# Performance work log

Measured on AMD Instinct MI355X. Metric: run time of the kernel, lower is better.

Reference implementation:

```python
import jax, jax.numpy as jnp
import numpy as np
from jax import lax

B, T, D, V, K = 32, 2048, 512, 1024, 3
COVERAGE_FLOOR = 0.05
LN_EPS = 1e-5


def _gelu(x):
    return jax.nn.gelu(x, approximate=False)  # torch F.gelu default is exact erf


def _causal_conv(h, w, b):
    # h: [B,T,D]; w: [D_out, D_in, K]; left-pad (K-1) for causality
    x = jnp.transpose(h, (0, 2, 1))  # [B,D,T]
    y = lax.conv_general_dilated(x, w, window_strides=(1,),
                                 padding=[(w.shape[-1] - 1, 0)],
                                 dimension_numbers=("NCH", "OIH", "NCH"))
    return jnp.transpose(y + b[None, :, None], (0, 2, 1))  # [B,T,D]


def _layer_norm(x, g, b):
    m = x.mean(-1, keepdims=True)
    v = ((x - m) ** 2).mean(-1, keepdims=True)
    return (x - m) / jnp.sqrt(v + LN_EPS) * g + b


def _masked_median(values, mask):
    # values, mask: [B,T]; torch median = lower middle = sorted[(n-1)//2]
    valid = mask > 0.5
    n = valid.sum(axis=1)  # [B]
    s = jnp.sort(jnp.where(valid, values, jnp.inf), axis=1)
    idx = jnp.clip((n - 1) // 2, 0, values.shape[1] - 1)
    med = jnp.take_along_axis(s, idx[:, None], axis=1)  # [B,1]
    return jnp.where((n > 0)[:, None], med, 0.0)


def _masked_mean(values, mask):
    denom = jnp.clip(mask.sum(axis=1, keepdims=True), 1.0, None)  # [B,1]
    return (values * mask[:, :, None]).sum(axis=1) / denom  # [B,D]


def _masked_std(values, mask, mean):
    denom = jnp.clip(mask.sum(axis=1, keepdims=True), 1.0, None)
    diff2 = (values - mean[:, None, :]) ** 2 * mask[:, :, None]
    return jnp.sqrt(diff2.sum(axis=1) / jnp.clip(denom, 1e-6, None) + 1e-6)


def setup_inputs() -> dict:
    key = jax.random.key(0)
    ks = jax.random.split(key, 16)
    s = 0.02
    return {
        "unit_ids": jax.random.randint(ks[0], (B, T), 0, V),
        "duration_obs": jax.random.uniform(ks[1], (B, T), jnp.float32, 0.01, 2.0),
        "mask": (jax.random.uniform(ks[2], (B, T)) > 0.3).astype(jnp.float32),
        "emb": jax.random.normal(ks[3], (V, D), jnp.float32) * s,
        "aux_w": jax.random.normal(ks[4], (D, 1), jnp.float32) * s,
        "aux_b": jnp.zeros((D,), jnp.float32),
        "conv1_w": jax.random.normal(ks[5], (D, D, K), jnp.float32) * s,
        "conv1_b": jnp.zeros((D,), jnp.float32),
        "conv2_w": jax.random.normal(ks[6], (D, D, K), jnp.float32) * s,
        "conv2_b": jnp.zeros((D,), jnp.float32),
        "ln_g": jnp.ones((D,), jnp.float32),
        "ln_b": jnp.zeros((D,), jnp.float32),
        "p1_w": jax.random.normal(ks[7], (D, 2 * D), jnp.float32) * s,
        "p1_b": jnp.zeros((D,), jnp.float32),
        "p2_w": jax.random.normal(ks[8], (D, D), jnp.float32) * s,
        "p2_b": jnp.zeros((D,), jnp.float32),
    }


def reference(unit_ids, duration_obs, mask, emb, aux_w, aux_b,
              conv1_w, conv1_b, conv2_w, conv2_b, ln_g, ln_b,
              p1_w, p1_b, p2_w, p2_b):
    mask = jnp.clip(mask.astype(jnp.float32), 0.0, 1.0)  # [B,T]
    logdur = jnp.log(jnp.clip(duration_obs.astype(jnp.float32), 1e-4, None)) * mask
    global_rate = _masked_median(logdur, mask)  # [B,1]
    ref_residual = (logdur - global_rate) * mask  # [B,T]

    # CausalStretchQueryEncoder
    hidden = emb[unit_ids] + (ref_residual[:, :, None] * aux_w[None, None, :, 0] + aux_b)
    hidden = _gelu(_causal_conv(hidden, conv1_w, conv1_b))
    hidden = _gelu(_causal_conv(hidden, conv2_w, conv2_b))
    hidden = _layer_norm(hidden, ln_g, ln_b) * mask[:, :, None]  # [B,T,D]

    mean = _masked_mean(hidden, mask)  # [B,D]
    std = _masked_std(hidden, mask, mean)  # [B,D]
    h = jnp.concatenate([mean, std], axis=-1)  # [B,2D]
    summary_state = jnp.tanh(_gelu(h @ p1_w.T + p1_b) @ p2_w.T + p2_b)  # [B,D]

    support_raw = mask.sum(axis=1, keepdims=True)  # [B,1]
    support = jnp.clip(support_raw, 1.0, None)
    summary_state = jnp.where(support_raw > 0.0, summary_state, 0.0)
    coverage = jnp.clip(support_raw / float(T), COVERAGE_FLOOR, None)

    residual_mean = (ref_residual * mask).sum(axis=1, keepdims=True) / support  # [B,1]
    residual_var = jnp.clip(((ref_residual - residual_mean) ** 2 * mask).sum(axis=1, keepdims=True) / support, 1e-4, None)
    attn = (mask / support)[:, :, None]  # [B,T,1]
    prompt_role_fit = residual_mean * jnp.ones_like(ref_residual) * mask  # [B,T]
    coeff_norm = jnp.linalg.norm(summary_state, axis=-1, keepdims=True)  # [B,1]

    return (global_rate, summary_state, residual_mean, residual_var, coverage,
            mask, logdur, ref_residual, attn, prompt_role_fit, coeff_norm)
```

## Files before the change

kernel.cpp:

```cpp
#include <hip/hip_runtime.h>
#include <hip/hip_bf16.h>
#include <math.h>

#define B_  32
#define T_  2048
#define D_  512
#define V_  1024
#define K_  3

typedef __attribute__((ext_vector_type(8))) short   short8;
typedef __attribute__((ext_vector_type(4))) float   floatx4;
typedef __attribute__((ext_vector_type(2))) long    longx2;

#define SCALE_H0 256.0f
#define SCALE_A  64.0f
#define SCALE_W  16.0f
#define INV1 (1.0f/(SCALE_H0*SCALE_W))
#define INV2 (1.0f/(SCALE_A*SCALE_W))

#define OFF0 0
#define OFF1 32
#define OFF2 16416
#define OFF3 16448
#define OFF4 16480
#define OFF5 16512
#define OFF6 82048
#define OFF7 147584
#define OFF8 213120
#define OFF9 278656
#define OFF10 344192

#define WS_RR     0
#define WS_SUP    262144
#define WS_PSUM   262272
#define WS_PSUMSQ 327808
#define WS_W1P    393344
#define WS_W2P    1212544
#define WS_H1     2031744
#define WS_S1     35618944
#define WS_NRM    35684480

__device__ __forceinline__ float clampf(float v, float lo, float hi) {
    v = (v > lo) ? v : lo;
    return (v < hi) ? v : hi;
}
__device__ __forceinline__ float gelu_exact(float v) {
    return 0.5f * v * (1.0f + erff(v * 0.70710678118654752440f));
}
__device__ __forceinline__ unsigned char f2fp8(float x) {
    int v = __builtin_amdgcn_cvt_pk_fp8_f32(x, x, 0, false);
    return (unsigned char)(v & 0xFF);
}
__device__ __forceinline__ int pk4fp8(float a, float b, float c, float d) {
    int p0 = __builtin_amdgcn_cvt_pk_fp8_f32(a, b, 0, false);
    int p1 = __builtin_amdgcn_cvt_pk_fp8_f32(c, d, 0, false);
    return (p1 << 16) | (p0 & 0xFFFF);
}

__device__ __forceinline__ float block_reduce_sum(float v, float* red, int tid) {
    __syncthreads();
    red[tid] = v;
    __syncthreads();
    for (int s = 128; s > 0; s >>= 1) {
        if (tid < s) red[tid] += red[tid + s];
        __syncthreads();
    }
    float r = red[0];
    __syncthreads();
    return r;
}

#define NB 2048
#define HLO (-9.3f)
#define HSC ((float)NB / 10.05f)
#define WLS 1544
__global__ __launch_bounds__(256) void init_kernel(
    const float* __restrict__ dur, const float* __restrict__ maskp,
    const float* __restrict__ w1, const float* __restrict__ w2,
    unsigned char* __restrict__ W1p, unsigned char* __restrict__ W2p,
    unsigned char* __restrict__ H1buf,
    float* __restrict__ rr_ws, float* __restrict__ sup_ws,
    float* __restrict__ psum, float* __restrict__ out)
{
    int tid = threadIdx.x;

    if (blockIdx.x >= 32) {
        __shared__ unsigned char Wl[2 * 16 * WLS];
        int ntg = blockIdx.x - 32;
        int lane = tid & 63, wave = tid >> 6;

        #pragma unroll
        for (int ws = 0; ws < 2; ++ws) {
            const float* wsrc = (ws ? w2 : w1) + (size_t)ntg * 16 * 1536;
            for (int i = tid; i < 6144; i += 256) {
                float4 v = ((const float4*)wsrc)[i];
                int col_local = i / 384;
                int pos = (i % 384) * 4;
                int word = pk4fp8(v.x * SCALE_W, v.y * SCALE_W,
                                  v.z * SCALE_W, v.w * SCALE_W);
                *(int*)(&Wl[(ws * 16 + col_local) * WLS + pos]) = word;
            }
        }
        __syncthreads();

        int cl = lane & 15, qq = lane >> 4;
        int pg = ntg >> 1, half = ntg & 1;
        #pragma unroll
        for (int ws = 0; ws < 2; ++ws) {
            unsigned char* dst = ws ? W2p : W1p;
            for (int s = wave; s < 48; s += 4) {
                int ci = s & 15, k = s >> 4;
                const unsigned char* row = &Wl[(ws * 16 + cl) * WLS];
                int kin = ci * 32 + qq * 8;
                unsigned char bb[8];
                #pragma unroll
                for (int e = 0; e < 8; ++e)
                    bb[e] = row[(kin + e) * 3 + k];
                *(double*)(dst + (((size_t)(s * 16 + pg) * 64 + lane) * 16
                                  + half * 8)) = *(double*)bb;
            }
        }

        int pid2 = ntg * 256 + tid;
        #pragma unroll
        for (int j = 0; j < 4; ++j) {
            int idx = pid2 + j * 8192;
            psum[idx] = 0.0f;
            int b = idx >> 10;
            int r = (idx >> 9) & 1;
            int d = idx & 511;
            H1buf[((size_t)b * 2050 + r) * 512 + d] = 0;
        }
        return;
    }

    __shared__ int   hist[NB];
    __shared__ int   csum[256];
    __shared__ float red[256];
    __shared__ float cand[128];
    __shared__ float nsh, medsh;
    __shared__ int   sh_tb, sh_cb, sh_candn;

    int b = blockIdx.x;
    const float* durb = dur + (size_t)b * T_;
    const float* mkb  = maskp + (size_t)b * T_;

    float ld[8], mk[8];
    int   bn[8];
    float cnt = 0.0f;
    #pragma unroll
    for (int i = 0; i < 8; ++i) hist[tid * 8 + i] = 0;
    __syncthreads();
    #pragma unroll
    for (int i = 0; i < 8; ++i) {
        int t = tid + i * 256;
        float m = clampf(mkb[t], 0.0f, 1.0f);
        float dv = durb[t];
        dv = (dv >= 1e-4f) ? dv : 1e-4f;
        float l = logf(dv) * m;
        ld[i] = l; mk[i] = m;
        int bin = (int)((l - HLO) * HSC);
        bin = (bin < 0) ? 0 : ((bin > NB - 1) ? NB - 1 : bin);
        bn[i] = bin;
        if (m > 0.5f) { cnt += 1.0f; atomicAdd(&hist[bin], 1); }
    }
    float n = block_reduce_sum(cnt, red, tid);
    if (tid == 0) { nsh = n; sh_candn = 0; medsh = 0.0f; }

    {
        int cs = 0;
        #pragma unroll
        for (int i = 0; i < 8; ++i) cs += hist[tid * 8 + i];
        csum[tid] = cs;
        __syncthreads();
        for (int off = 1; off < 256; off <<= 1) {
            int v = (tid >= off) ? csum[tid - off] : 0;
            __syncthreads();
            csum[tid] += v;
            __syncthreads();
        }
    }
    int ni = (int)(n + 0.5f);
    int k  = (ni > 0) ? ((ni - 1) >> 1) : 0;
    {
        int prevIncl = (tid > 0) ? csum[tid - 1] : 0;
        if (ni > 0 && k >= prevIncl && k < csum[tid]) {
            int cum = prevIncl, tb = tid * 8;
            #pragma unroll
            for (int i = 0; i < 8; ++i) {
                int c = hist[tid * 8 + i];
                if (k < cum + c) { tb = tid * 8 + i; break; }
                cum += c;
            }
            sh_tb = tb; sh_cb = cum;
        }
    }
    __syncthreads();
    if (ni > 0) {
        int tb = sh_tb;
        #pragma unroll
        for (int i = 0; i < 8; ++i) {
            if (mk[i] > 0.5f && bn[i] == tb) {
                int p = atomicAdd(&sh_candn, 1);
                if (p < 128) cand[p] = ld[i];
            }
        }
    }
    __syncthreads();
    if (tid == 0 && ni > 0) {
        int m = k - sh_cb;
        int cn = (sh_candn < 128) ? sh_candn : 128;
        float best = cand[0];
        for (int i = 0; i < cn; ++i) {
            int rank = 0;
            for (int j = 0; j < cn; ++j)
                rank += (cand[j] < cand[i]) || (cand[j] == cand[i] && j < i);
            if (rank == m) { best = cand[i]; break; }
        }
        medsh = best;
    }
    __syncthreads();
    float med = (ni > 0) ? medsh : 0.0f;
    med = clampf(med, -20.0f, 20.0f);

    float denom = (n > 1.0f) ? n : 1.0f;
    float rv[8];
    float ssum = 0.0f;
    #pragma unroll
    for (int i = 0; i < 8; ++i) { rv[i] = (ld[i] - med) * mk[i]; ssum += rv[i]; }
    float rsum = block_reduce_sum(ssum, red, tid);
    float rm = clampf(rsum / denom, -40.0f, 40.0f);

    float vsum_l = 0.0f;
    #pragma unroll
    for (int i = 0; i < 8; ++i) { float dd = rv[i] - rm; vsum_l += dd * dd * mk[i]; }
    float vsum = block_reduce_sum(vsum_l, red, tid);
    float var = clampf(vsum / denom, 1e-4f, 1e4f);

    float inv_sup = 1.0f / denom;
    #pragma unroll
    for (int i = 0; i < 8; ++i) {
        int t = tid + i * 256;
        size_t o = (size_t)b * T_ + t;
        out[OFF5 + o] = mk[i];
        out[OFF6 + o] = ld[i];
        out[OFF7 + o] = rv[i];
        out[OFF8 + o] = mk[i] * inv_sup;
        out[OFF9 + o] = rm * mk[i];
        rr_ws[o] = rv[i];
    }
    if (tid == 0) {
        out[OFF0 + b] = med;
        out[OFF2 + b] = rm;
        out[OFF3 + b] = var;
        float cov = n * (1.0f / (float)T_);
        out[OFF4 + b] = (cov > 0.05f) ? cov : 0.05f;
        sup_ws[b] = n;
    }
}

#define H0S 520
__global__ __launch_bounds__(256, 3) void conv1g_kernel(
    const int* __restrict__ ids, const float* __restrict__ rr,
    const float* __restrict__ emb,
    const float* __restrict__ aux_w, const float* __restrict__ aux_b,
    const unsigned char* __restrict__ W1p, const float* __restrict__ bias1,
    unsigned char* __restrict__ H1buf)
{
    __shared__ __align__(16) unsigned char H0s[66 * H0S];
    __shared__ int   lid[66];
    __shared__ float lrr[66];

    int tile = blockIdx.x;
    int b    = blockIdx.y;
    int r0   = tile << 6;
    int tid  = threadIdx.x;
    int wave = tid >> 6, lane = tid & 63;
    int q = lane >> 4, m16 = lane & 15;

    if (tid < 66) {
        int t = r0 - 2 + tid;
        bool v = (t >= 0);
        lid[tid] = v ? ids[b * T_ + t] : -1;
        lrr[tid] = v ? rr[(size_t)b * T_ + t] : 0.0f;
    }
    __syncthreads();

    {
        int c4 = tid & 127;
        float4 aw = *(const float4*)(aux_w + c4 * 4);
        float4 ab = *(const float4*)(aux_b + c4 * 4);
        int rbase = tid >> 7;
        for (int j = 0; j < 33; ++j) {
            int row = rbase + j * 2;
            int id = lid[row];
            int word = 0;
            if (id >= 0) {
                float vr = lrr[row];
                float4 e = *(const float4*)(emb + (size_t)id * D_ + c4 * 4);
                word = pk4fp8((e.x + vr * aw.x + ab.x) * SCALE_H0,
                              (e.y + vr * aw.y + ab.y) * SCALE_H0,
                              (e.z + vr * aw.z + ab.z) * SCALE_H0,
                              (e.w + vr * aw.w + ab.w) * SCALE_H0);
            }
            *(int*)(&H0s[row * H0S + c4 * 4]) = word;
        }
    }
    __syncthreads();

    unsigned char* Ob = H1buf + ((size_t)b * 2050 + 2 + r0) * 512;

#define CONV1_PHASE(FR0, FR1, SS)                                              \
    {   int k1 = (SS) >> 4, ci = (SS) & 15;                                    \
        _Pragma("unroll")                                                      \
        for (int mt = 0; mt < 4; ++mt) {                                       \
            long afr = *(const long*)(&H0s[(mt * 16 + m16 + k1) * H0S + ci * 32 + q * 8]); \
            acc[mt][0] = __builtin_amdgcn_mfma_f32_16x16x32_fp8_fp8(afr, FR0[0], acc[mt][0], 0, 0, 0); \
            acc[mt][1] = __builtin_amdgcn_mfma_f32_16x16x32_fp8_fp8(afr, FR0[1], acc[mt][1], 0, 0, 0); \
            acc[mt][2] = __builtin_amdgcn_mfma_f32_16x16x32_fp8_fp8(afr, FR1[0], acc[mt][2], 0, 0, 0); \
            acc[mt][3] = __builtin_amdgcn_mfma_f32_16x16x32_fp8_fp8(afr, FR1[1], acc[mt][3], 0, 0, 0); \
        } }

    #pragma unroll
    for (int nh = 0; nh < 2; ++nh) {
        floatx4 acc[4][4];
        #pragma unroll
        for (int i = 0; i < 4; ++i)
            #pragma unroll
            for (int j = 0; j < 4; ++j)
                acc[i][j] = (floatx4){0.f, 0.f, 0.f, 0.f};

        const longx2* wp0 = (const longx2*)W1p
                          + ((size_t)(0 * 16 + nh * 8 + wave * 2 + 0) * 64 + lane);
        const longx2* wp1 = wp0 + 64;

        longx2 fA0 = wp0[0],                  fA1 = wp1[0];
        longx2 fB0 = wp0[(size_t)1 * 1024],   fB1 = wp1[(size_t)1 * 1024];
        longx2 fC0, fC1, fD0, fD1;

        #pragma unroll 1
        for (int s = 0; s < 48; s += 4) {
            fC0 = wp0[(size_t)(s + 2) * 1024]; fC1 = wp1[(size_t)(s + 2) * 1024];
            CONV1_PHASE(fA0, fA1, s)
            fD0 = wp0[(size_t)(s + 3) * 1024]; fD1 = wp1[(size_t)(s + 3) * 1024];
            CONV1_PHASE(fB0, fB1, s + 1)
            fA0 = wp0[(size_t)(s + 4) * 1024]; fA1 = wp1[(size_t)(s + 4) * 1024];
            CONV1_PHASE(fC0, fC1, s + 2)
            fB0 = wp0[(size_t)(s + 5) * 1024]; fB1 = wp1[(size_t)(s + 5) * 1024];
            CONV1_PHASE(fD0, fD1, s + 3)
        }

        #pragma unroll
        for (int mt = 0; mt < 4; ++mt) {
            #pragma unroll
            for (int nt = 0; nt < 4; ++nt) {
                int col = nh * 256 + wave * 64 + nt * 16 + m16;
                float bsv = bias1[col];
                #pragma unroll
                for (int r = 0; r < 4; ++r) {
                    int row = mt * 16 + q * 4 + r;
                    float v = gelu_exact(acc[mt][nt][r] * INV1 + bsv) * SCALE_A;
                    Ob[(size_t)row * 512 + col] = f2fp8(v);
                }
            }
        }
    }
#undef CONV1_PHASE
}

#define H1S 520
__global__ __launch_bounds__(256, 2) void conv2ln_kernel(
    const unsigned char* __restrict__ H1buf, const unsigned char* __restrict__ W2p,
    const float* __restrict__ bias2,
    const float* __restrict__ ln_g, const float* __restrict__ ln_b,
    const float* __restrict__ maskp,
    float* __restrict__ psum, float* __restrict__ psumsq)
{
    __shared__ __align__(16) unsigned char H1s[34 * H1S];
    __shared__ float mrow[32];
    __shared__ float part[32][4][2];
    __shared__ float tot[32][2];
    __shared__ float colsum[512][2];

    int tile = blockIdx.x;
    int b    = blockIdx.y;
    int r0   = tile << 5;
    int tid  = threadIdx.x;
    int wave = tid >> 6, lane = tid & 63;
    int q = lane >> 4, m16 = lane & 15;
    int nbase = wave << 7;

    const unsigned char* src = H1buf + ((size_t)b * 2050 + r0) * 512;
    for (int g = tid; g < 34 * 32; g += 256) {
        int row = g >> 5, h = g & 31;
        *(float4*)(&H1s[row * H1S + h * 16]) = *(const float4*)(src + (size_t)row * 512 + h * 16);
    }
    if (tid < 32)
        mrow[tid] = clampf(maskp[(size_t)b * T_ + r0 + tid], 0.0f, 1.0f);
    __syncthreads();

    floatx4 acc[2][8];
    #pragma unroll
    for (int i = 0; i < 2; ++i)
        #pragma unroll
        for (int j = 0; j < 8; ++j)
            acc[i][j] = (floatx4){0.f, 0.f, 0.f, 0.f};

    const longx2* wq0 = (const longx2*)W2p + ((size_t)(wave * 4 + 0) * 64 + lane);
    const longx2* wq1 = (const longx2*)W2p + ((size_t)(wave * 4 + 1) * 64 + lane);
    const longx2* wq2 = (const longx2*)W2p + ((size_t)(wave * 4 + 2) * 64 + lane);
    const longx2* wq3 = (const longx2*)W2p + ((size_t)(wave * 4 + 3) * 64 + lane);

#define C2_PHASE(F0, F1, F2, F3, SS)                                           \
    {   int k2 = (SS) >> 4, ci = (SS) & 15;                                    \
        _Pragma("unroll")                                                      \
        for (int mt = 0; mt < 2; ++mt) {                                       \
            long afr = *(const long*)(&H1s[(mt * 16 + m16 + k2) * H1S + ci * 32 + q * 8]); \
            acc[mt][0] = __builtin_amdgcn_mfma_f32_16x16x32_fp8_fp8(afr, F0[0], acc[mt][0], 0, 0, 0); \
            acc[mt][1] = __builtin_amdgcn_mfma_f32_16x16x32_fp8_fp8(afr, F0[1], acc[mt][1], 0, 0, 0); \
            acc[mt][2] = __builtin_amdgcn_mfma_f32_16x16x32_fp8_fp8(afr, F1[0], acc[mt][2], 0, 0, 0); \
            acc[mt][3] = __builtin_amdgcn_mfma_f32_16x16x32_fp8_fp8(afr, F1[1], acc[mt][3], 0, 0, 0); \
            acc[mt][4] = __builtin_amdgcn_mfma_f32_16x16x32_fp8_fp8(afr, F2[0], acc[mt][4], 0, 0, 0); \
            acc[mt][5] = __builtin_amdgcn_mfma_f32_16x16x32_fp8_fp8(afr, F2[1], acc[mt][5], 0, 0, 0); \
            acc[mt][6] = __builtin_amdgcn_mfma_f32_16x16x32_fp8_fp8(afr, F3[0], acc[mt][6], 0, 0, 0); \
            acc[mt][7] = __builtin_amdgcn_mfma_f32_16x16x32_fp8_fp8(afr, F3[1], acc[mt][7], 0, 0, 0); \
        } }

    longx2 fA0 = wq0[0], fA1 = wq1[0], fA2 = wq2[0], fA3 = wq3[0];
    longx2 fB0 = wq0[(size_t)1 * 1024], fB1 = wq1[(size_t)1 * 1024];
    longx2 fB2 = wq2[(size_t)1 * 1024], fB3 = wq3[(size_t)1 * 1024];
    longx2 fC0, fC1, fC2, fC3, fD0, fD1, fD2, fD3;

    #pragma unroll 1
    for (int s = 0; s < 48; s += 4) {
        fC0 = wq0[(size_t)(s + 2) * 1024]; fC1 = wq1[(size_t)(s + 2) * 1024];
        fC2 = wq2[(size_t)(s + 2) * 1024]; fC3 = wq3[(size_t)(s + 2) * 1024];
        C2_PHASE(fA0, fA1, fA2, fA3, s)
        fD0 = wq0[(size_t)(s + 3) * 1024]; fD1 = wq1[(size_t)(s + 3) * 1024];
        fD2 = wq2[(size_t)(s + 3) * 1024]; fD3 = wq3[(size_t)(s + 3) * 1024];
        C2_PHASE(fB0, fB1, fB2, fB3, s + 1)
        fA0 = wq0[(size_t)(s + 4) * 1024]; fA1 = wq1[(size_t)(s + 4) * 1024];
        fA2 = wq2[(size_t)(s + 4) * 1024]; fA3 = wq3[(size_t)(s + 4) * 1024];
        C2_PHASE(fC0, fC1, fC2, fC3, s + 2)
        fB0 = wq0[(size_t)(s + 5) * 1024]; fB1 = wq1[(size_t)(s + 5) * 1024];
        fB2 = wq2[(size_t)(s + 5) * 1024]; fB3 = wq3[(size_t)(s + 5) * 1024];
        C2_PHASE(fD0, fD1, fD2, fD3, s + 3)
    }
#undef C2_PHASE

    #pragma unroll
    for (int mt = 0; mt < 2; ++mt)
        #pragma unroll
        for (int nt = 0; nt < 8; ++nt) {
            int col = nbase + nt * 16 + m16;
            float bsv = bias2[col];
            #pragma unroll
            for (int r = 0; r < 4; ++r)
                acc[mt][nt][r] = gelu_exact(acc[mt][nt][r] * INV2 + bsv);
        }

    #pragma unroll
    for (int mt = 0; mt < 2; ++mt) {
        #pragma unroll
        for (int r = 0; r < 4; ++r) {
            float rs = 0.f, rq = 0.f;
            #pragma unroll
            for (int nt = 0; nt < 8; ++nt) {
                float v = acc[mt][nt][r];
                rs += v; rq += v * v;
            }
            rs += __shfl_xor(rs, 1);  rq += __shfl_xor(rq, 1);
            rs += __shfl_xor(rs, 2);  rq += __shfl_xor(rq, 2);
            rs += __shfl_xor(rs, 4);  rq += __shfl_xor(rq, 4);
            rs += __shfl_xor(rs, 8);  rq += __shfl_xor(rq, 8);
            if (m16 == 0) {
                int row = mt * 16 + q * 4 + r;
                part[row][wave][0] = rs;
                part[row][wave][1] = rq;
            }
        }
    }
    __syncthreads();
    if (tid < 64) {
        int row = tid >> 1, j = tid & 1;
        tot[row][j] = part[row][0][j] + part[row][1][j] + part[row][2][j] + part[row][3][j];
    }
    __syncthreads();

    float meanv[2][4], rstdv[2][4];
    #pragma unroll
    for (int mt = 0; mt < 2; ++mt)
        #pragma unroll
        for (int r = 0; r < 4; ++r) {
            int row = mt * 16 + q * 4 + r;
            float m = tot[row][0] * (1.0f / D_);
            float var = tot[row][1] * (1.0f / D_) - m * m;
            meanv[mt][r] = m;
            rstdv[mt][r] = rsqrtf((var > 0.0f ? var : 0.0f) + 1e-5f);
        }

    float cs[8], cq[8];
    #pragma unroll
    for (int nt = 0; nt < 8; ++nt) { cs[nt] = 0.f; cq[nt] = 0.f; }
    #pragma unroll
    for (int mt = 0; mt < 2; ++mt) {
        #pragma unroll
        for (int r = 0; r < 4; ++r) {
            int row = mt * 16 + q * 4 + r;
            float mk = mrow[row];
            float m = meanv[mt][r], rs = rstdv[mt][r];
            #pragma unroll
            for (int nt = 0; nt < 8; ++nt) {
                int col = nbase + nt * 16 + m16;
                float xn = ((acc[mt][nt][r] - m) * rs * ln_g[col] + ln_b[col]) * mk;
                cs[nt] += xn;
                cq[nt] += xn * xn;
            }
        }
    }
    #pragma unroll
    for (int nt = 0; nt < 8; ++nt) {
        cs[nt] += __shfl_xor(cs[nt], 16);  cq[nt] += __shfl_xor(cq[nt], 16);
        cs[nt] += __shfl_xor(cs[nt], 32);  cq[nt] += __shfl_xor(cq[nt], 32);
    }
    if (lane < 16) {
        #pragma unroll
        for (int nt = 0; nt < 8; ++nt) {
            int col = nbase + nt * 16 + m16;
            colsum[col][0] = cs[nt];
            colsum[col][1] = cq[nt];
        }
    }
    __syncthreads();
    for (int i = tid; i < 512; i += 256) {
        atomicAdd(&psum[(size_t)b * D_ + i], colsum[i][0]);
        atomicAdd(&psumsq[(size_t)b * D_ + i], colsum[i][1]);
    }
}

__global__ __launch_bounds__(128) void mlp1_kernel(
    const float* __restrict__ psum, const float* __restrict__ psumsq,
    const float* __restrict__ sup_ws,
    const float* __restrict__ p1w, const float* __restrict__ p1b,
    float* __restrict__ s1_ws, float* __restrict__ nrm_ws)
{
    int b = blockIdx.x, jt = blockIdx.y;
    int tid = threadIdx.x;
    __shared__ float h[2 * D_];

    float n = sup_ws[b];
    float denom = (n > 1.0f) ? n : 1.0f;
    for (int i = tid; i < D_; i += 128) {
        float S = psum[(size_t)b * D_ + i];
        float Q = psumsq[(size_t)b * D_ + i];
        float mean = S / denom;
        float msum = Q - 2.0f * mean * S + n * mean * mean;
        float arg = msum / denom + 1e-6f;
        h[i] = mean;
        h[D_ + i] = sqrtf((arg > 0.0f) ? arg : 0.0f);
    }
    if (jt == 0 && tid == 0) nrm_ws[b] = 0.0f;
    __syncthreads();

    int d  = jt * 64 + (tid >> 1);
    int kh = tid & 1;
    float z = (kh == 0) ? p1b[d] : 0.0f;
    const float4* w4 = (const float4*)(p1w + (size_t)d * (2 * D_) + kh * D_);
    const float*  hh = &h[kh * D_];
    for (int jj = 0; jj < D_ / 4; ++jj) {
        float4 wv = w4[jj];
        z += hh[jj * 4 + 0] * wv.x + hh[jj * 4 + 1] * wv.y
           + hh[jj * 4 + 2] * wv.z + hh[jj * 4 + 3] * wv.w;
    }
    z += __shfl_xor(z, 1);
    if (kh == 0) s1_ws[(size_t)b * D_ + d] = gelu_exact(z);
}

__global__ __launch_bounds__(128) void mlp2_kernel(
    const float* __restrict__ s1_ws, const float* __restrict__ sup_ws,
    const float* __restrict__ p2w, const float* __restrict__ p2b,
    float* __restrict__ nrm_ws, float* __restrict__ out)
{
    int b = blockIdx.x, jt = blockIdx.y;
    int tid = threadIdx.x;
    __shared__ float s1[D_];
    __shared__ float red[128];

    for (int i = tid; i < D_; i += 128) s1[i] = s1_ws[(size_t)b * D_ + i];
    __syncthreads();

    int d  = jt * 64 + (tid >> 1);
    int kh = tid & 1;
    float z2 = (kh == 0) ? p2b[d] : 0.0f;
    const float4* w24 = (const float4*)(p2w + (size_t)d * D_ + kh * 256);
    const float*  ss  = &s1[kh * 256];
    for (int jj = 0; jj < 64; ++jj) {
        float4 wv = w24[jj];
        z2 += ss[jj * 4 + 0] * wv.x + ss[jj * 4 + 1] * wv.y
            + ss[jj * 4 + 2] * wv.z + ss[jj * 4 + 3] * wv.w;
    }
    z2 += __shfl_xor(z2, 1);
    float nsup = sup_ws[b];
    float st = tanhf(z2);
    if (!(nsup > 0.0f)) st = 0.0f;
    if (kh == 0) out[OFF1 + (size_t)b * D_ + d] = st;

    red[tid] = (kh == 0) ? st * st : 0.0f;
    __syncthreads();
    for (int s = 64; s > 0; s >>= 1) {
        if (tid < s) red[tid] += red[tid + s];
        __syncthreads();
    }
    if (tid == 0) atomicAdd(&nrm_ws[b], red[0]);
}

__global__ __launch_bounds__(64) void mlp3_kernel(
    const float* __restrict__ nrm_ws, float* __restrict__ out)
{
    int b = threadIdx.x;
    if (b < B_) out[OFF10 + b] = sqrtf(nrm_ws[b]);
}

extern "C" void kernel_launch(void* const* d_in, const int* in_sizes, int n_in,
                              void* d_out, int out_size, void* d_ws, size_t ws_size,
                              hipStream_t stream) {
    (void)in_sizes; (void)n_in; (void)out_size; (void)ws_size;
    const int*   unit_ids = (const int*)d_in[0];
    const float* dur      = (const float*)d_in[1];
    const float* mask     = (const float*)d_in[2];
    const float* emb      = (const float*)d_in[3];
    const float* aux_w    = (const float*)d_in[4];
    const float* aux_b    = (const float*)d_in[5];
    const float* conv1_w  = (const float*)d_in[6];
    const float* conv1_b  = (const float*)d_in[7];
    const float* conv2_w  = (const float*)d_in[8];
    const float* conv2_b  = (const float*)d_in[9];
    const float* ln_g     = (const float*)d_in[10];
    const float* ln_b     = (const float*)d_in[11];
    const float* p1_w     = (const float*)d_in[12];
    const float* p1_b     = (const float*)d_in[13];
    const float* p2_w     = (const float*)d_in[14];
    const float* p2_b     = (const float*)d_in[15];
    float* out = (float*)d_out;

    char* ws = (char*)d_ws;
    float*          rr     = (float*)(ws + WS_RR);
    float*          sup    = (float*)(ws + WS_SUP);
    float*          psum   = (float*)(ws + WS_PSUM);
    float*          psumsq = (float*)(ws + WS_PSUMSQ);
    unsigned char*  W1p    = (unsigned char*)(ws + WS_W1P);
    unsigned char*  W2p    = (unsigned char*)(ws + WS_W2P);
    unsigned char*  H1buf  = (unsigned char*)(ws + WS_H1);
    float*          s1_ws  = (float*)(ws + WS_S1);
    float*          nrm_ws = (float*)(ws + WS_NRM);

    init_kernel<<<dim3(64), dim3(256), 0, stream>>>(
        dur, mask, conv1_w, conv2_w, W1p, W2p, H1buf, rr, sup, psum, out);
    conv1g_kernel<<<dim3(32, 32), dim3(256), 0, stream>>>(
        unit_ids, rr, emb, aux_w, aux_b, W1p, conv1_b, H1buf);
    conv2ln_kernel<<<dim3(64, 32), dim3(256), 0, stream>>>(
        H1buf, W2p, conv2_b, ln_g, ln_b, mask, psum, psumsq);
    mlp1_kernel<<<dim3(32, 8), dim3(128), 0, stream>>>(
        psum, psumsq, sup, p1_w, p1_b, s1_ws, nrm_ws);
    mlp2_kernel<<<dim3(32, 8), dim3(128), 0, stream>>>(
        s1_ws, sup, p2_w, p2_b, nrm_ws, out);
    mlp3_kernel<<<dim3(1), dim3(64), 0, stream>>>(nrm_ws, out);
}
```

Measured before the change: 321.7 us.

## Split weight packing across more blocks, raise conv2 occupancy, fold norm kernel

Weight packing in init now gives each block only one of the two weight tensors, so it runs on 64 packing blocks instead of 32 with half the shared memory each. The conv2+LayerNorm kernel drops its hand-written four-stage register prefetch pipeline for a simple loop unrolled by two, and raises its launch-bounds occupancy target from 2 to 3 blocks per SM. The final sqrt-norm kernel is removed: a per-batch counter lets the last mlp2 block finish the norm, saving one launch. Losing the explicit prefetch may expose global-load latency in conv2 unless the higher occupancy hides it.

```diff
diff --git a/kernel.cpp b/kernel.cpp
--- a/kernel.cpp
+++ b/kernel.cpp
@@ -39,6 +39,7 @@
 #define WS_H1     2031744
 #define WS_S1     35618944
 #define WS_NRM    35684480
+#define WS_CNT    35684608
 
 __device__ __forceinline__ float clampf(float v, float lo, float hi) {
     v = (v > lo) ? v : lo;
@@ -85,46 +86,41 @@
     int tid = threadIdx.x;
 
     if (blockIdx.x >= 32) {
-        __shared__ unsigned char Wl[2 * 16 * WLS];
-        int ntg = blockIdx.x - 32;
+        __shared__ unsigned char Wl[16 * WLS];
+        int pb  = blockIdx.x - 32;
+        int ws  = pb & 1;
+        int ntg = pb >> 1;
         int lane = tid & 63, wave = tid >> 6;
 
-        #pragma unroll
-        for (int ws = 0; ws < 2; ++ws) {
-            const float* wsrc = (ws ? w2 : w1) + (size_t)ntg * 16 * 1536;
-            for (int i = tid; i < 6144; i += 256) {
-                float4 v = ((const float4*)wsrc)[i];
-                int col_local = i / 384;
-                int pos = (i % 384) * 4;
-                int word = pk4fp8(v.x * SCALE_W, v.y * SCALE_W,
-                                  v.z * SCALE_W, v.w * SCALE_W);
-                *(int*)(&Wl[(ws * 16 + col_local) * WLS + pos]) = word;
-            }
+        const float* wsrc = (ws ? w2 : w1) + (size_t)ntg * 16 * 1536;
+        for (int i = tid; i < 6144; i += 256) {
+            float4 v = ((const float4*)wsrc)[i];
+            int col_local = i / 384;
+            int pos = (i % 384) * 4;
+            int word = pk4fp8(v.x * SCALE_W, v.y * SCALE_W,
+                              v.z * SCALE_W, v.w * SCALE_W);
+            *(int*)(&Wl[col_local * WLS + pos]) = word;
         }
         __syncthreads();
 
         int cl = lane & 15, qq = lane >> 4;
         int pg = ntg >> 1, half = ntg & 1;
-        #pragma unroll
-        for (int ws = 0; ws < 2; ++ws) {
-            unsigned char* dst = ws ? W2p : W1p;
-            for (int s = wave; s < 48; s += 4) {
-                int ci = s & 15, k = s >> 4;
-                const unsigned char* row = &Wl[(ws * 16 + cl) * WLS];
-                int kin = ci * 32 + qq * 8;
-                unsigned char bb[8];
-                #pragma unroll
-                for (int e = 0; e < 8; ++e)
-                    bb[e] = row[(kin + e) * 3 + k];
-                *(double*)(dst + (((size_t)(s * 16 + pg) * 64 + lane) * 16
-                                  + half * 8)) = *(double*)bb;
-            }
-        }
-
-        int pid2 = ntg * 256 + tid;
-        #pragma unroll
-        for (int j = 0; j < 4; ++j) {
-            int idx = pid2 + j * 8192;
+        unsigned char* dst = ws ? W2p : W1p;
+        for (int s = wave; s < 48; s += 4) {
+            int ci = s & 15, k = s >> 4;
+            const unsigned char* row = &Wl[cl * WLS];
+            int kin = ci * 32 + qq * 8;
+            unsigned char bb[8];
+            #pragma unroll
+            for (int e = 0; e < 8; ++e)
+                bb[e] = row[(kin + e) * 3 + k];
+            *(double*)(dst + (((size_t)(s * 16 + pg) * 64 + lane) * 16
+                              + half * 8)) = *(double*)bb;
+        }
+
+        #pragma unroll
+        for (int j = 0; j < 2; ++j) {
+            int idx = pb * 512 + j * 256 + tid;
             psum[idx] = 0.0f;
             int b = idx >> 10;
             int r = (idx >> 9) & 1;
@@ -369,7 +365,7 @@
 }
 
 #define H1S 520
-__global__ __launch_bounds__(256, 2) void conv2ln_kernel(
+__global__ __launch_bounds__(256, 3) void conv2ln_kernel(
     const unsigned char* __restrict__ H1buf, const unsigned char* __restrict__ W2p,
     const float* __restrict__ bias2,
     const float* __restrict__ ln_g, const float* __restrict__ ln_b,
@@ -406,47 +402,28 @@
         for (int j = 0; j < 8; ++j)
             acc[i][j] = (floatx4){0.f, 0.f, 0.f, 0.f};
 
-    const longx2* wq0 = (const longx2*)W2p + ((size_t)(wave * 4 + 0) * 64 + lane);
-    const longx2* wq1 = (const longx2*)W2p + ((size_t)(wave * 4 + 1) * 64 + lane);
-    const longx2* wq2 = (const longx2*)W2p + ((size_t)(wave * 4 + 2) * 64 + lane);
-    const longx2* wq3 = (const longx2*)W2p + ((size_t)(wave * 4 + 3) * 64 + lane);
-
-#define C2_PHASE(F0, F1, F2, F3, SS)                                           \
-    {   int k2 = (SS) >> 4, ci = (SS) & 15;                                    \
-        _Pragma("unroll")                                                      \
-        for (int mt = 0; mt < 2; ++mt) {                                       \
-            long afr = *(const long*)(&H1s[(mt * 16 + m16 + k2) * H1S + ci * 32 + q * 8]); \
-            acc[mt][0] = __builtin_amdgcn_mfma_f32_16x16x32_fp8_fp8(afr, F0[0], acc[mt][0], 0, 0, 0); \
-            acc[mt][1] = __builtin_amdgcn_mfma_f32_16x16x32_fp8_fp8(afr, F0[1], acc[mt][1], 0, 0, 0); \
-            acc[mt][2] = __builtin_amdgcn_mfma_f32_16x16x32_fp8_fp8(afr, F1[0], acc[mt][2], 0, 0, 0); \
-            acc[mt][3] = __builtin_amdgcn_mfma_f32_16x16x32_fp8_fp8(afr, F1[1], acc[mt][3], 0, 0, 0); \
-            acc[mt][4] = __builtin_amdgcn_mfma_f32_16x16x32_fp8_fp8(afr, F2[0], acc[mt][4], 0, 0, 0); \
-            acc[mt][5] = __builtin_amdgcn_mfma_f32_16x16x32_fp8_fp8(afr, F2[1], acc[mt][5], 0, 0, 0); \
-            acc[mt][6] = __builtin_amdgcn_mfma_f32_16x16x32_fp8_fp8(afr, F3[0], acc[mt][6], 0, 0, 0); \
-            acc[mt][7] = __builtin_amdgcn_mfma_f32_16x16x32_fp8_fp8(afr, F3[1], acc[mt][7], 0, 0, 0); \
-        } }
-
-    longx2 fA0 = wq0[0], fA1 = wq1[0], fA2 = wq2[0], fA3 = wq3[0];
-    longx2 fB0 = wq0[(size_t)1 * 1024], fB1 = wq1[(size_t)1 * 1024];
-    longx2 fB2 = wq2[(size_t)1 * 1024], fB3 = wq3[(size_t)1 * 1024];
-    longx2 fC0, fC1, fC2, fC3, fD0, fD1, fD2, fD3;
-
-    #pragma unroll 1
-    for (int s = 0; s < 48; s += 4) {
-        fC0 = wq0[(size_t)(s + 2) * 1024]; fC1 = wq1[(size_t)(s + 2) * 1024];
-        fC2 = wq2[(size_t)(s + 2) * 1024]; fC3 = wq3[(size_t)(s + 2) * 1024];
-        C2_PHASE(fA0, fA1, fA2, fA3, s)
-        fD0 = wq0[(size_t)(s + 3) * 1024]; fD1 = wq1[(size_t)(s + 3) * 1024];
-        fD2 = wq2[(size_t)(s + 3) * 1024]; fD3 = wq3[(size_t)(s + 3) * 1024];
-        C2_PHASE(fB0, fB1, fB2, fB3, s + 1)
-        fA0 = wq0[(size_t)(s + 4) * 1024]; fA1 = wq1[(size_t)(s + 4) * 1024];
-        fA2 = wq2[(size_t)(s + 4) * 1024]; fA3 = wq3[(size_t)(s + 4) * 1024];
-        C2_PHASE(fC0, fC1, fC2, fC3, s + 2)
-        fB0 = wq0[(size_t)(s + 5) * 1024]; fB1 = wq1[(size_t)(s + 5) * 1024];
-        fB2 = wq2[(size_t)(s + 5) * 1024]; fB3 = wq3[(size_t)(s + 5) * 1024];
-        C2_PHASE(fD0, fD1, fD2, fD3, s + 3)
-    }
-#undef C2_PHASE
+    const longx2* wq = (const longx2*)W2p + ((size_t)(wave * 4) * 64 + lane);
+
+    #pragma unroll 2
+    for (int s = 0; s < 48; ++s) {
+        int k2 = s >> 4, ci = s & 15;
+        longx2 f0 = wq[(size_t)s * 1024];
+        longx2 f1 = wq[(size_t)s * 1024 + 64];
+        longx2 f2 = wq[(size_t)s * 1024 + 128];
+        longx2 f3 = wq[(size_t)s * 1024 + 192];
+        #pragma unroll
+        for (int mt = 0; mt < 2; ++mt) {
+            long afr = *(const long*)(&H1s[(mt * 16 + m16 + k2) * H1S + ci * 32 + q * 8]);
+            acc[mt][0] = __builtin_amdgcn_mfma_f32_16x16x32_fp8_fp8(afr, f0[0], acc[mt][0], 0, 0, 0);
+            acc[mt][1] = __builtin_amdgcn_mfma_f32_16x16x32_fp8_fp8(afr, f0[1], acc[mt][1], 0, 0, 0);
+            acc[mt][2] = __builtin_amdgcn_mfma_f32_16x16x32_fp8_fp8(afr, f1[0], acc[mt][2], 0, 0, 0);
+            acc[mt][3] = __builtin_amdgcn_mfma_f32_16x16x32_fp8_fp8(afr, f1[1], acc[mt][3], 0, 0, 0);
+            acc[mt][4] = __builtin_amdgcn_mfma_f32_16x16x32_fp8_fp8(afr, f2[0], acc[mt][4], 0, 0, 0);
+            acc[mt][5] = __builtin_amdgcn_mfma_f32_16x16x32_fp8_fp8(afr, f2[1], acc[mt][5], 0, 0, 0);
+            acc[mt][6] = __builtin_amdgcn_mfma_f32_16x16x32_fp8_fp8(afr, f3[0], acc[mt][6], 0, 0, 0);
+            acc[mt][7] = __builtin_amdgcn_mfma_f32_16x16x32_fp8_fp8(afr, f3[1], acc[mt][7], 0, 0, 0);
+        }
+    }
 
     #pragma unroll
     for (int mt = 0; mt < 2; ++mt)
@@ -542,7 +519,8 @@
     const float* __restrict__ psum, const float* __restrict__ psumsq,
     const float* __restrict__ sup_ws,
     const float* __restrict__ p1w, const float* __restrict__ p1b,
-    float* __restrict__ s1_ws, float* __restrict__ nrm_ws)
+    float* __restrict__ s1_ws, float* __restrict__ nrm_ws,
+    int* __restrict__ cnt_ws)
 {
     int b = blockIdx.x, jt = blockIdx.y;
     int tid = threadIdx.x;
@@ -559,7 +537,7 @@
         h[i] = mean;
         h[D_ + i] = sqrtf((arg > 0.0f) ? arg : 0.0f);
     }
-    if (jt == 0 && tid == 0) nrm_ws[b] = 0.0f;
+    if (jt == 0 && tid == 0) { nrm_ws[b] = 0.0f; cnt_ws[b] = 0; }
     __syncthreads();
 
     int d  = jt * 64 + (tid >> 1);
@@ -579,7 +557,8 @@
 __global__ __launch_bounds__(128) void mlp2_kernel(
     const float* __restrict__ s1_ws, const float* __restrict__ sup_ws,
     const float* __restrict__ p2w, const float* __restrict__ p2b,
-    float* __restrict__ nrm_ws, float* __restrict__ out)
+    float* __restrict__ nrm_ws, int* __restrict__ cnt_ws,
+    float* __restrict__ out)
 {
     int b = blockIdx.x, jt = blockIdx.y;
     int tid = threadIdx.x;
@@ -611,14 +590,15 @@
         if (tid < s) red[tid] += red[tid + s];
         __syncthreads();
     }
-    if (tid == 0) atomicAdd(&nrm_ws[b], red[0]);
-}
-
-__global__ __launch_bounds__(64) void mlp3_kernel(
-    const float* __restrict__ nrm_ws, float* __restrict__ out)
-{
-    int b = threadIdx.x;
-    if (b < B_) out[OFF10 + b] = sqrtf(nrm_ws[b]);
+    if (tid == 0) {
+        atomicAdd(&nrm_ws[b], red[0]);
+        __threadfence();
+        int old = atomicAdd(&cnt_ws[b], 1);
+        if (old == 7) {
+            float nv = atomicAdd(&nrm_ws[b], 0.0f);
+            out[OFF10 + b] = sqrtf(nv);
+        }
+    }
 }
 
 extern "C" void kernel_launch(void* const* d_in, const int* in_sizes, int n_in,
@@ -653,16 +633,16 @@
     unsigned char*  H1buf  = (unsigned char*)(ws + WS_H1);
     float*          s1_ws  = (float*)(ws + WS_S1);
     float*          nrm_ws = (float*)(ws + WS_NRM);
-
-    init_kernel<<<dim3(64), dim3(256), 0, stream>>>(
+    int*            cnt_ws = (int*)(ws + WS_CNT);
+
+    init_kernel<<<dim3(96), dim3(256), 0, stream>>>(
         dur, mask, conv1_w, conv2_w, W1p, W2p, H1buf, rr, sup, psum, out);
     conv1g_kernel<<<dim3(32, 32), dim3(256), 0, stream>>>(
         unit_ids, rr, emb, aux_w, aux_b, W1p, conv1_b, H1buf);
     conv2ln_kernel<<<dim3(64, 32), dim3(256), 0, stream>>>(
         H1buf, W2p, conv2_b, ln_g, ln_b, mask, psum, psumsq);
     mlp1_kernel<<<dim3(32, 8), dim3(128), 0, stream>>>(
-        psum, psumsq, sup, p1_w, p1_b, s1_ws, nrm_ws);
+        psum, psumsq, sup, p1_w, p1_b, s1_ws, nrm_ws, cnt_ws);
     mlp2_kernel<<<dim3(32, 8), dim3(128), 0, stream>>>(
-        s1_ws, sup, p2_w, p2_b, nrm_ws, out);
-    mlp3_kernel<<<dim3(1), dim3(64), 0, stream>>>(nrm_ws, out);
-}
+        s1_ws, sup, p2_w, p2_b, nrm_ws, cnt_ws, out);
+}
```

After: 378.3 us. 17.6% more time.
